# Performance work log

Hardware: AMD Instinct MI355X
Metric: run time of the kernel (lower is better)

Reference implementation:

```python
import jax, jax.numpy as jnp
import numpy as np

H = 1024      # hidden_dim
C = 151       # len(obj_classes)
E = 200       # embed_dim (GloVe)
DIN = 2048    # inputs_dim
T = 32        # timesteps
B = 128       # batch size (uniform packed lengths)


def setup_inputs() -> dict:
    key = jax.random.key(0)
    ks = jax.random.split(key, 8)
    sequence_tensor = jax.random.normal(ks[0], (T * B, DIN), dtype=jnp.float32) * 0.1
    labels = jax.random.randint(ks[1], (T * B,), 0, C).astype(jnp.int64)
    embed = jax.random.normal(ks[2], (C + 1, E), dtype=jnp.float32) * 0.1   # obj_embed.weight
    Wi = jax.random.normal(ks[3], (DIN + E, 6 * H), dtype=jnp.float32) * 0.02  # input_linearity
    bi = jnp.zeros((6 * H,), dtype=jnp.float32)
    Ws = jax.random.normal(ks[4], (H, 5 * H), dtype=jnp.float32) * 0.02        # state_linearity
    bs = jnp.zeros((5 * H,), dtype=jnp.float32)
    Wo = jax.random.normal(ks[5], (H, C), dtype=jnp.float32) * 0.02            # out_obj
    bo = jnp.zeros((C,), dtype=jnp.float32)
    return {"sequence_tensor": sequence_tensor, "labels": labels, "embed": embed,
            "Wi": Wi, "bi": bi, "Ws": Ws, "bs": bs, "Wo": Wo, "bo": bo,
            "batch_size": B}


def reference(sequence_tensor, embed, Wi, bi, Ws, bs, Wo, bo, labels, batch_size):
    b = int(batch_size)
    t = sequence_tensor.shape[0] // b
    x = sequence_tensor.reshape(t, b, -1)          # [T, B, DIN] packed timestep-major
    lab = labels.reshape(t, b)                     # [T, B]
    h0 = jnp.zeros((b, H), dtype=sequence_tensor.dtype)
    c0 = jnp.zeros((b, H), dtype=sequence_tensor.dtype)
    e0 = jnp.broadcast_to(embed[0], (b, E))        # 'start' embedding

    def step(carry, inp):
        h, c, pe = carry
        xt, lt = inp
        ti = jnp.concatenate([xt, pe], axis=1)     # [B, DIN+E]
        pi = ti @ Wi + bi                          # [B, 6H]
        ps = h @ Ws + bs                           # [B, 5H]

        def gate(k):
            return pi[:, k * H:(k + 1) * H] + ps[:, k * H:(k + 1) * H]

        i_g = jax.nn.sigmoid(gate(0))
        f_g = jax.nn.sigmoid(gate(1))
        m_i = jnp.tanh(gate(2))
        o_g = jax.nn.sigmoid(gate(3))
        c_new = i_g * m_i + f_g * c
        out = o_g * jnp.tanh(c_new)
        hw = jax.nn.sigmoid(gate(4))
        h_new = hw * out + (1.0 - hw) * pi[:, 5 * H:6 * H]  # highway

        pred = h_new @ Wo + bo                     # [B, C]
        nzp = jnp.argmax(pred[:, 1:], axis=1) + 1  # best non-bg class
        l2e = jnp.where(lt == 0, nzp.astype(lt.dtype), lt)
        pe_new = embed[l2e + 1]                    # feedback embedding
        return (h_new, c_new, pe_new), (pred, l2e)

    _, (dists, comms) = jax.lax.scan(step, (h0, c0, e0), (x, lab))
    return dists.reshape(t * b, C), comms.reshape(t * b)
```

## Files before the change

kernel.cpp:

```cpp
#include <hip/hip_runtime.h>
#include <math.h>

#define H    1024
#define C    151
#define E    200
#define DIN  2048
#define T    32
#define B    128
#define SIXH  (6*H)
#define FIVEH (5*H)
#define KTOT  DIN
#define NEMB  (C+1)
#define NWG   160
#define COLS  32
#define GUARD (1 << 20)

typedef _Float16 f16x8 __attribute__((ext_vector_type(8)));
typedef _Float16 f16x4 __attribute__((ext_vector_type(4)));
typedef float    f32x4 __attribute__((ext_vector_type(4)));

#define GLOAD_LDS16(g, l) __builtin_amdgcn_global_load_lds( \
    (const __attribute__((address_space(1))) unsigned int*)(g), \
    (__attribute__((address_space(3))) unsigned int*)(l), 16, 0, 0)

__device__ __forceinline__ void gbar(int* slots, int tid, int val) {
    __syncthreads();
    if (tid == 0)
        __hip_atomic_fetch_add(&slots[blockIdx.x * 16], 1,
                               __ATOMIC_ACQ_REL, __HIP_MEMORY_SCOPE_AGENT);
    int ok, guard = 0;
    do {
        int v = val;
        if (tid < NWG)
            v = __hip_atomic_load(&slots[tid * 16],
                                  __ATOMIC_RELAXED, __HIP_MEMORY_SCOPE_AGENT);
        ok = __syncthreads_and(v >= val);
        if (!ok) __builtin_amdgcn_s_sleep(1);
    } while (!ok && ++guard < GUARD);
    __builtin_amdgcn_fence(__ATOMIC_ACQUIRE, "agent");
}

__global__ void init_kernel(float* h, float* c, _Float16* hhi, _Float16* hlo,
                            int* eidx, int* bar) {
    int i = blockIdx.x * blockDim.x + threadIdx.x;
    if (i < B * H) {
        h[i] = 0.f; c[i] = 0.f;
        hhi[i] = (_Float16)0.f; hlo[i] = (_Float16)0.f;
    }
    if (i < B) eidx[i] = 0;
    if (i < NWG * 16) bar[i] = 0;
}

__global__ void cvt_x(const float* __restrict__ X, _Float16* __restrict__ hi,
                      _Float16* __restrict__ lo) {
    size_t i = ((size_t)blockIdx.x * 256 + threadIdx.x) * 4;
    float4 v = *(const float4*)(X + i);
    f16x4 h, l;
    h.x = (_Float16)v.x; l.x = (_Float16)(v.x - (float)h.x);
    h.y = (_Float16)v.y; l.y = (_Float16)(v.y - (float)h.y);
    h.z = (_Float16)v.z; l.z = (_Float16)(v.z - (float)h.z);
    h.w = (_Float16)v.w; l.w = (_Float16)(v.w - (float)h.w);
    *(f16x4*)(hi + i) = h;
    *(f16x4*)(lo + i) = l;
}

template<int KR, int NC>
__global__ void cvt_wT(const float* __restrict__ W, _Float16* __restrict__ hi,
                       _Float16* __restrict__ lo) {
    __shared__ float tile[32][33];
    int n0 = blockIdx.x * 32, k0 = blockIdx.y * 32;
    int tx = threadIdx.x & 31, ty = threadIdx.x >> 5;
    #pragma unroll
    for (int i = 0; i < 4; ++i) {
        int k = ty + i * 8;
        tile[k][tx] = W[(size_t)(k0 + k) * NC + n0 + tx];
    }
    __syncthreads();
    #pragma unroll
    for (int i = 0; i < 4; ++i) {
        int n = ty + i * 8;
        float v = tile[tx][n];
        _Float16 h = (_Float16)v;
        size_t o = (size_t)(n0 + n) * KR + k0 + tx;
        hi[o] = h;
        lo[o] = (_Float16)(v - (float)h);
    }
}

__global__ void cvt_woT(const float* __restrict__ Wo, float* __restrict__ WoT) {
    int k = blockIdx.x * 256 + threadIdx.x;
    for (int c = 0; c < C; ++c)
        WoT[(size_t)c * H + k] = Wo[(size_t)k * C + c];
}

__global__ void etab_kernel(const float* __restrict__ embed,
                            const float* __restrict__ Wi,
                            float* __restrict__ Etab) {
    int n = blockIdx.x * 256 + threadIdx.x;
    int k = blockIdx.y;
    const float* wp = Wi + (size_t)DIN * SIXH + n;
    const float* ep = embed + k * E;
    float acc = 0.f;
    #pragma unroll 8
    for (int e = 0; e < E; ++e)
        acc = fmaf(ep[e], wp[(size_t)e * SIXH], acc);
    Etab[(size_t)k * SIXH + n] = acc;
}

__global__ __launch_bounds__(256) void big_gemm_mfma(
    const _Float16* __restrict__ Ahi, const _Float16* __restrict__ Alo,
    const _Float16* __restrict__ Bhi, const _Float16* __restrict__ Blo,
    const float* __restrict__ bi, float* __restrict__ P)
{
    __shared__ __align__(16) _Float16 sAh[128 * 32];
    __shared__ __align__(16) _Float16 sAl[128 * 32];
    __shared__ __align__(16) _Float16 sBh[128 * 32];
    __shared__ __align__(16) _Float16 sBl[128 * 32];
    const int tid = threadIdx.x;
    const int n0 = blockIdx.x * 128;
    const int m0 = blockIdx.y * 128;
    const int lane = tid & 63, w = tid >> 6;
    const int wm = (w >> 1) * 64, wn = (w & 1) * 64;
    const int lr = lane & 15, lq = lane >> 4;

    f32x4 acc[4][4];
    #pragma unroll
    for (int i = 0; i < 4; ++i)
        #pragma unroll
        for (int j = 0; j < 4; ++j)
            acc[i][j] = (f32x4){0.f, 0.f, 0.f, 0.f};

    const int row0 = tid >> 2;
    const int kc = tid & 3;
    const int kcs = kc ^ ((row0 >> 1) & 3);
    const int sw = (lq ^ ((lr >> 1) & 3)) * 8;

    for (int k0 = 0; k0 < KTOT; k0 += 32) {
        #pragma unroll
        for (int i = 0; i < 2; ++i) {
            int row = row0 + i * 64;
            size_t ga = (size_t)(m0 + row) * KTOT + k0 + kcs * 8;
            size_t gb = (size_t)(n0 + row) * KTOT + k0 + kcs * 8;
            int loff = (i * 256 + tid) * 8;
            GLOAD_LDS16(Ahi + ga, sAh + loff);
            GLOAD_LDS16(Alo + ga, sAl + loff);
            GLOAD_LDS16(Bhi + gb, sBh + loff);
            GLOAD_LDS16(Blo + gb, sBl + loff);
        }
        __syncthreads();
        f16x8 ah[4], al[4], bh[4], bl[4];
        #pragma unroll
        for (int i = 0; i < 4; ++i) {
            ah[i] = *(const f16x8*)&sAh[(wm + i * 16 + lr) * 32 + sw];
            al[i] = *(const f16x8*)&sAl[(wm + i * 16 + lr) * 32 + sw];
            bh[i] = *(const f16x8*)&sBh[(wn + i * 16 + lr) * 32 + sw];
            bl[i] = *(const f16x8*)&sBl[(wn + i * 16 + lr) * 32 + sw];
        }
        #pragma unroll
        for (int i = 0; i < 4; ++i)
            #pragma unroll
            for (int j = 0; j < 4; ++j) {
                acc[i][j] = __builtin_amdgcn_mfma_f32_16x16x32_f16(ah[i], bh[j], acc[i][j], 0, 0, 0);
                acc[i][j] = __builtin_amdgcn_mfma_f32_16x16x32_f16(ah[i], bl[j], acc[i][j], 0, 0, 0);
                acc[i][j] = __builtin_amdgcn_mfma_f32_16x16x32_f16(al[i], bh[j], acc[i][j], 0, 0, 0);
            }
        __syncthreads();
    }
    #pragma unroll
    for (int i = 0; i < 4; ++i)
        #pragma unroll
        for (int j = 0; j < 4; ++j) {
            int gcol = n0 + wn + j * 16 + lr;
            float bv = bi[gcol];
            #pragma unroll
            for (int r = 0; r < 4; ++r) {
                int grow = m0 + wm + i * 16 + lq * 4 + r;
                P[(size_t)grow * SIXH + gcol] = acc[i][j][r] + bv;
            }
        }
}

__global__ __launch_bounds__(256, 1) void fused_loop(
    const float* __restrict__ P,
    const float* __restrict__ Etab,
    const float* __restrict__ bs,
    const _Float16* __restrict__ WsThi,
    const _Float16* __restrict__ WsTlo,
    _Float16* __restrict__ hhi,
    _Float16* __restrict__ hlo,
    float* __restrict__ ps,
    const float* __restrict__ WoT,
    const float* __restrict__ bo,
    const int* __restrict__ labels,
    float* __restrict__ dists,
    float* __restrict__ comms,
    int* bar)
{
    __shared__ __align__(16) _Float16 sBh[COLS * H];
    __shared__ __align__(16) _Float16 sBl[COLS * H];
    __shared__ __align__(16) float hs[H];
    __shared__ float vals[256];
    __shared__ int   idxs[256];
    __shared__ int   s_eidx;

    const int wg  = blockIdx.x;
    const int tid = threadIdx.x;
    const int n0  = wg * COLS;
    const int lane = tid & 63, w = tid >> 6;
    const int lr = lane & 15, lq = lane >> 4;

    for (int gi = tid; gi < COLS * (H / 8); gi += 256) {
        int col = gi >> 7;
        int kg  = gi & 127;
        int dst = (col * (H * 2) + kg * 16) ^ ((col & 7) << 4);
        *(f16x8*)((char*)sBh + dst) = *(const f16x8*)&WsThi[(size_t)(n0 + col) * H + kg * 8];
        *(f16x8*)((char*)sBl + dst) = *(const f16x8*)&WsTlo[(size_t)(n0 + col) * H + kg * 8];
    }

    float creg[4] = {0.f, 0.f, 0.f, 0.f};
    float bsr[4][5];
    if (wg < B) {
        #pragma unroll
        for (int jj = 0; jj < 4; ++jj)
            #pragma unroll
            for (int k = 0; k < 5; ++k)
                bsr[jj][k] = bs[k * H + jj * 256 + tid];
    }
    if (tid == 0) s_eidx = 0;
    __syncthreads();

    const int mrow0 = w * 32;
    int bval = 0;

    for (int t = 0; t < T; ++t) {
        int eidx_cur = s_eidx;

        f32x4 acc[2][2];
        #pragma unroll
        for (int i = 0; i < 2; ++i)
            #pragma unroll
            for (int j = 0; j < 2; ++j)
                acc[i][j] = (f32x4){0.f, 0.f, 0.f, 0.f};

        #pragma unroll 4
        for (int k0 = 0; k0 < H; k0 += 32) {
            f16x8 ah[2], al[2], bh[2], bl[2];
            #pragma unroll
            for (int i = 0; i < 2; ++i) {
                size_t ho = (size_t)(mrow0 + i * 16 + lr) * H + k0 + lq * 8;
                ah[i] = *(const f16x8*)&hhi[ho];
                al[i] = *(const f16x8*)&hlo[ho];
            }
            #pragma unroll
            for (int j = 0; j < 2; ++j) {
                int col = j * 16 + lr;
                int off = (col * (H * 2) + (k0 + lq * 8) * 2) ^ ((col & 7) << 4);
                bh[j] = *(const f16x8*)((const char*)sBh + off);
                bl[j] = *(const f16x8*)((const char*)sBl + off);
            }
            #pragma unroll
            for (int i = 0; i < 2; ++i)
                #pragma unroll
                for (int j = 0; j < 2; ++j) {
                    acc[i][j] = __builtin_amdgcn_mfma_f32_16x16x32_f16(ah[i], bh[j], acc[i][j], 0, 0, 0);
                    acc[i][j] = __builtin_amdgcn_mfma_f32_16x16x32_f16(ah[i], bl[j], acc[i][j], 0, 0, 0);
                    acc[i][j] = __builtin_amdgcn_mfma_f32_16x16x32_f16(al[i], bh[j], acc[i][j], 0, 0, 0);
                }
        }
        #pragma unroll
        for (int i = 0; i < 2; ++i)
            #pragma unroll
            for (int j = 0; j < 2; ++j)
                #pragma unroll
                for (int r = 0; r < 4; ++r)
                    ps[(size_t)(mrow0 + i * 16 + lq * 4 + r) * FIVEH + n0 + j * 16 + lr] = acc[i][j][r];

        float pf[4][6], pe[4][6];
        if (wg < B) {
            const float* prow = P + (size_t)(t * B + wg) * SIXH;
            const float* erow = Etab + (size_t)eidx_cur * SIXH;
            #pragma unroll
            for (int jj = 0; jj < 4; ++jj)
                #pragma unroll
                for (int k = 0; k < 6; ++k) {
                    pf[jj][k] = prow[k * H + jj * 256 + tid];
                    pe[jj][k] = erow[k * H + jj * 256 + tid];
                }
        }

        ++bval; gbar(bar, tid, bval);

        if (wg < B) {
            const int b = wg;
            const float* psr = ps + (size_t)b * FIVEH;
            #pragma unroll
            for (int jj = 0; jj < 4; ++jj) {
                int j = jj * 256 + tid;
                float gv[5];
                #pragma unroll
                for (int k = 0; k < 5; ++k)
                    gv[k] = pf[jj][k] + pe[jj][k] + psr[k * H + j] + bsr[jj][k];
                float pi5 = pf[jj][5] + pe[jj][5];
                float ig = 1.f / (1.f + expf(-gv[0]));
                float fg = 1.f / (1.f + expf(-gv[1]));
                float mi = tanhf(gv[2]);
                float og = 1.f / (1.f + expf(-gv[3]));
                float hw = 1.f / (1.f + expf(-gv[4]));
                float cn = ig * mi + fg * creg[jj];
                float out = og * tanhf(cn);
                float hn = hw * out + (1.f - hw) * pi5;
                creg[jj] = cn;
                hs[j] = hn;
                _Float16 hh = (_Float16)hn;
                hhi[(size_t)b * H + j] = hh;
                hlo[(size_t)b * H + j] = (_Float16)(hn - (float)hh);
            }
            __syncthreads();
            float predv = 0.f;
            if (tid < C) {
                const float* wp = WoT + (size_t)tid * H;
                float a0 = bo[tid], a1 = 0.f, a2 = 0.f, a3 = 0.f;
                #pragma unroll 4
                for (int k = 0; k < H; k += 4) {
                    float4 w4 = *(const float4*)&wp[k];
                    float4 h4 = *(const float4*)&hs[k];
                    a0 = fmaf(h4.x, w4.x, a0);
                    a1 = fmaf(h4.y, w4.y, a1);
                    a2 = fmaf(h4.z, w4.z, a2);
                    a3 = fmaf(h4.w, w4.w, a3);
                }
                predv = (a0 + a1) + (a2 + a3);
                dists[(size_t)(t * B + b) * C + tid] = predv;
            }
            vals[tid] = (tid >= 1 && tid < C) ? predv : -1e30f;
            idxs[tid] = tid;
            __syncthreads();
            for (int s = 128; s > 0; s >>= 1) {
                if (tid < s) {
                    float v2 = vals[tid + s];
                    int   i2 = idxs[tid + s];
                    if (v2 > vals[tid] || (v2 == vals[tid] && i2 < idxs[tid])) {
                        vals[tid] = v2;
                        idxs[tid] = i2;
                    }
                }
                __syncthreads();
            }
            if (tid == 0) {
                int nzp = idxs[0];
                int lt = labels[t * B + b];
                int comm = (lt == 0) ? nzp : lt;
                comms[t * B + b] = (float)comm;
                s_eidx = comm + 1;
            }
        }
        ++bval; gbar(bar, tid, bval);
    }
}

__global__ __launch_bounds__(256) void ps_mfma(
    const _Float16* __restrict__ Ahi, const _Float16* __restrict__ Alo,
    const _Float16* __restrict__ Bhi, const _Float16* __restrict__ Blo,
    float* __restrict__ ps)
{
    __shared__ __align__(16) _Float16 sAh[64 * 32];
    __shared__ __align__(16) _Float16 sAl[64 * 32];
    __shared__ __align__(16) _Float16 sBh[64 * 32];
    __shared__ __align__(16) _Float16 sBl[64 * 32];
    const int tid = threadIdx.x;
    const int n0 = blockIdx.x * 64;
    const int m0 = blockIdx.y * 64;
    const int lane = tid & 63, w = tid >> 6;
    const int wm = (w >> 1) * 32, wn = (w & 1) * 32;
    const int lr = lane & 15, lq = lane >> 4;

    f32x4 acc[2][2];
    #pragma unroll
    for (int i = 0; i < 2; ++i)
        #pragma unroll
        for (int j = 0; j < 2; ++j)
            acc[i][j] = (f32x4){0.f, 0.f, 0.f, 0.f};

    const int row = tid >> 2;
    const int kc = tid & 3;

    for (int k0 = 0; k0 < H; k0 += 32) {
        size_t ga = (size_t)(m0 + row) * H + k0 + kc * 8;
        size_t gb = (size_t)(n0 + row) * H + k0 + kc * 8;
        int loff = tid * 8;
        GLOAD_LDS16(Ahi + ga, sAh + loff);
        GLOAD_LDS16(Alo + ga, sAl + loff);
        GLOAD_LDS16(Bhi + gb, sBh + loff);
        GLOAD_LDS16(Blo + gb, sBl + loff);
        __syncthreads();
        f16x8 ah[2], al[2], bh[2], bl[2];
        #pragma unroll
        for (int i = 0; i < 2; ++i) {
            ah[i] = *(const f16x8*)&sAh[(wm + i * 16 + lr) * 32 + lq * 8];
            al[i] = *(const f16x8*)&sAl[(wm + i * 16 + lr) * 32 + lq * 8];
            bh[i] = *(const f16x8*)&sBh[(wn + i * 16 + lr) * 32 + lq * 8];
            bl[i] = *(const f16x8*)&sBl[(wn + i * 16 + lr) * 32 + lq * 8];
        }
        #pragma unroll
        for (int i = 0; i < 2; ++i)
            #pragma unroll
            for (int j = 0; j < 2; ++j) {
                acc[i][j] = __builtin_amdgcn_mfma_f32_16x16x32_f16(ah[i], bh[j], acc[i][j], 0, 0, 0);
                acc[i][j] = __builtin_amdgcn_mfma_f32_16x16x32_f16(ah[i], bl[j], acc[i][j], 0, 0, 0);
                acc[i][j] = __builtin_amdgcn_mfma_f32_16x16x32_f16(al[i], bh[j], acc[i][j], 0, 0, 0);
            }
        __syncthreads();
    }
    #pragma unroll
    for (int i = 0; i < 2; ++i)
        #pragma unroll
        for (int j = 0; j < 2; ++j) {
            int gcol = n0 + wn + j * 16 + lr;
            #pragma unroll
            for (int r = 0; r < 4; ++r) {
                int grow = m0 + wm + i * 16 + lq * 4 + r;
                ps[(size_t)grow * FIVEH + gcol] = acc[i][j][r];
            }
        }
}

__global__ void gate_kernel(const float* __restrict__ P,
                            const float* __restrict__ Etab,
                            const float* __restrict__ ps,
                            const float* __restrict__ bs,
                            const int* __restrict__ eidx,
                            float* __restrict__ h,
                            float* __restrict__ c,
                            _Float16* __restrict__ hhi,
                            _Float16* __restrict__ hlo,
                            int t) {
    int j = blockIdx.x * 256 + threadIdx.x;
    int b = blockIdx.y;
    const float* prow = P + (size_t)(t * B + b) * SIXH;
    const float* erow = Etab + (size_t)eidx[b] * SIXH;
    const float* psr  = ps + (size_t)b * FIVEH;
    float g[5];
    #pragma unroll
    for (int k = 0; k < 5; ++k) {
        int col = k * H + j;
        g[k] = prow[col] + erow[col] + psr[col] + bs[col];
    }
    float pi5 = prow[5 * H + j] + erow[5 * H + j];
    float ig = 1.f / (1.f + expf(-g[0]));
    float fg = 1.f / (1.f + expf(-g[1]));
    float mi = tanhf(g[2]);
    float og = 1.f / (1.f + expf(-g[3]));
    float hw = 1.f / (1.f + expf(-g[4]));
    float cv = c[b * H + j];
    float cn = ig * mi + fg * cv;
    float out = og * tanhf(cn);
    float hn = hw * out + (1.f - hw) * pi5;
    c[b * H + j] = cn;
    h[b * H + j] = hn;
    _Float16 hh = (_Float16)hn;
    hhi[b * H + j] = hh;
    hlo[b * H + j] = (_Float16)(hn - (float)hh);
}

__global__ void pred_kernel(const float* __restrict__ h,
                            const float* __restrict__ Wo,
                            const float* __restrict__ bo,
                            const int* __restrict__ labels,
                            float* __restrict__ dists,
                            float* __restrict__ comms,
                            int* __restrict__ eidx,
                            int t) {
    __shared__ float hsb[H];
    __shared__ float vals[256];
    __shared__ int   idxs[256];
    int tid = threadIdx.x;
    int b = blockIdx.x;
    for (int i = tid; i < H / 4; i += 256)
        *(float4*)&hsb[i * 4] = *(const float4*)&h[b * H + i * 4];
    __syncthreads();
    float pred = 0.f;
    if (tid < C) {
        pred = bo[tid];
        #pragma unroll 8
        for (int k = 0; k < H; ++k)
            pred = fmaf(hsb[k], Wo[k * C + tid], pred);
        dists[(size_t)(t * B + b) * C + tid] = pred;
    }
    vals[tid] = (tid >= 1 && tid < C) ? pred : -1e30f;
    idxs[tid] = tid;
    __syncthreads();
    for (int s = 128; s > 0; s >>= 1) {
        if (tid < s) {
            float v2 = vals[tid + s];
            int   i2 = idxs[tid + s];
            if (v2 > vals[tid] || (v2 == vals[tid] && i2 < idxs[tid])) {
                vals[tid] = v2;
                idxs[tid] = i2;
            }
        }
        __syncthreads();
    }
    if (tid == 0) {
        int nzp = idxs[0];
        int lt = labels[t * B + b];
        int comm = (lt == 0) ? nzp : lt;
        comms[t * B + b] = (float)comm;
        eidx[b] = comm + 1;
    }
}

extern "C" void kernel_launch(void* const* d_in, const int* in_sizes, int n_in,
                              void* d_out, int out_size, void* d_ws, size_t ws_size,
                              hipStream_t stream) {
    const float* X      = (const float*)d_in[0];
    const int*   labels = (const int*)  d_in[1];
    const float* embed  = (const float*)d_in[2];
    const float* Wi     = (const float*)d_in[3];
    const float* bi     = (const float*)d_in[4];
    const float* Ws     = (const float*)d_in[5];
    const float* bs     = (const float*)d_in[6];
    const float* Wo     = (const float*)d_in[7];
    const float* bo     = (const float*)d_in[8];

    char* w = (char*)d_ws;
    float* P      = (float*)w;              w += (size_t)T * B * SIXH * 4;
    float* Etab   = (float*)w;              w += (size_t)NEMB * SIXH * 4;
    float* ps     = (float*)w;              w += (size_t)B * FIVEH * 4;
    float* h      = (float*)w;              w += (size_t)B * H * 4;
    float* c      = (float*)w;              w += (size_t)B * H * 4;
    _Float16* hhi = (_Float16*)w;           w += (size_t)B * H * 2;
    _Float16* hlo = (_Float16*)w;           w += (size_t)B * H * 2;
    int* eidx     = (int*)w;                w += 512;
    int* bar      = (int*)w;                w += 16384;
    _Float16* Xhi = (_Float16*)w;           w += (size_t)T * B * KTOT * 2;
    _Float16* Xlo = (_Float16*)w;           w += (size_t)T * B * KTOT * 2;
    _Float16* WiThi = (_Float16*)w;         w += (size_t)SIXH * KTOT * 2;
    _Float16* WiTlo = (_Float16*)w;         w += (size_t)SIXH * KTOT * 2;
    _Float16* WsThi = (_Float16*)w;         w += (size_t)FIVEH * H * 2;
    _Float16* WsTlo = (_Float16*)w;         w += (size_t)FIVEH * H * 2;
    float* WoT    = (float*)Xhi;

    float* dists = (float*)d_out;
    float* comms = dists + (size_t)T * B * C;

    init_kernel<<<512, 256, 0, stream>>>(h, c, hhi, hlo, eidx, bar);
    cvt_x<<<(T * B * KTOT) / (256 * 4), 256, 0, stream>>>(X, Xhi, Xlo);
    cvt_wT<KTOT, SIXH><<<dim3(SIXH / 32, KTOT / 32), 256, 0, stream>>>(Wi, WiThi, WiTlo);
    cvt_wT<H, FIVEH><<<dim3(FIVEH / 32, H / 32), 256, 0, stream>>>(Ws, WsThi, WsTlo);
    etab_kernel<<<dim3(SIXH / 256, NEMB), 256, 0, stream>>>(embed, Wi, Etab);
    big_gemm_mfma<<<dim3(SIXH / 128, (T * B) / 128), 256, 0, stream>>>(Xhi, Xlo, WiThi, WiTlo, bi, P);
    cvt_woT<<<dim3(H / 256), 256, 0, stream>>>(Wo, WoT);

    void* args[] = {(void*)&P, (void*)&Etab, (void*)&bs, (void*)&WsThi, (void*)&WsTlo,
                    (void*)&hhi, (void*)&hlo, (void*)&ps, (void*)&WoT, (void*)&bo,
                    (void*)&labels, (void*)&dists, (void*)&comms, (void*)&bar};
    hipError_t err = hipLaunchCooperativeKernel((void*)fused_loop, dim3(NWG), dim3(256),
                                                args, 0, stream);
    if (err != hipSuccess) {
        for (int t = 0; t < T; ++t) {
            ps_mfma<<<dim3(FIVEH / 64, B / 64), 256, 0, stream>>>(hhi, hlo, WsThi, WsTlo, ps);
            gate_kernel<<<dim3(H / 256, B), 256, 0, stream>>>(P, Etab, ps, bs, eidx, h, c, hhi, hlo, t);
            pred_kernel<<<B, 256, 0, stream>>>(h, Wo, bo, labels, dists, comms, eidx, t);
        }
    }
}
```

Measured before the change: 2.443 ms.

## Split grid barrier into arrive/wait and double-buffer hidden-state loads

The grid barrier is split into separate arrive and wait phases. Each block now signals arrival as soon as it has written its new h, then computes the output projection and argmax before it waits, so that per-row tail work overlaps with barrier latency. The recurrent MFMA loop is also restructured into a manually double-buffered schedule: global loads of the hi/lo h fragments for the next 128-wide K chunk are issued while the current chunk is computed. The cost is higher register pressure from holding two sets of buffered fragments.

```diff
diff --git a/kernel.cpp b/kernel.cpp
--- a/kernel.cpp
+++ b/kernel.cpp
@@ -23,11 +23,13 @@
     (const __attribute__((address_space(1))) unsigned int*)(g), \
     (__attribute__((address_space(3))) unsigned int*)(l), 16, 0, 0)
 
-__device__ __forceinline__ void gbar(int* slots, int tid, int val) {
+__device__ __forceinline__ void gbar_arrive(int* slots, int tid) {
     __syncthreads();
     if (tid == 0)
         __hip_atomic_fetch_add(&slots[blockIdx.x * 16], 1,
                                __ATOMIC_ACQ_REL, __HIP_MEMORY_SCOPE_AGENT);
+}
+__device__ __forceinline__ void gbar_wait(int* slots, int tid, int val) {
     int ok, guard = 0;
     do {
         int v = val;
@@ -179,6 +181,32 @@
             }
         }
 }
+
+#define H_LOAD(Wa, Wl, kbase)                                                  \
+    _Pragma("unroll") for (int p = 0; p < 4; ++p)                              \
+    _Pragma("unroll") for (int i = 0; i < 2; ++i) {                            \
+        size_t ho = (size_t)(mrow0 + i * 16 + lr) * H + (kbase) + p * 32 + lq * 8; \
+        Wa[p][i] = *(const f16x8*)&hhi[ho];                                    \
+        Wl[p][i] = *(const f16x8*)&hlo[ho];                                    \
+    }
+
+#define H_COMP(Wa, Wl, kbase)                                                  \
+    _Pragma("unroll") for (int p = 0; p < 4; ++p) {                            \
+        const int k0 = (kbase) + p * 32;                                       \
+        f16x8 bh[2], bl[2];                                                    \
+        _Pragma("unroll") for (int j = 0; j < 2; ++j) {                        \
+            int col = j * 16 + lr;                                             \
+            int off = (col * (H * 2) + (k0 + lq * 8) * 2) ^ ((col & 7) << 4);  \
+            bh[j] = *(const f16x8*)((const char*)sBh + off);                   \
+            bl[j] = *(const f16x8*)((const char*)sBl + off);                   \
+        }                                                                      \
+        _Pragma("unroll") for (int i = 0; i < 2; ++i)                          \
+        _Pragma("unroll") for (int j = 0; j < 2; ++j) {                        \
+            acc[i][j] = __builtin_amdgcn_mfma_f32_16x16x32_f16(Wa[p][i], bh[j], acc[i][j], 0, 0, 0); \
+            acc[i][j] = __builtin_amdgcn_mfma_f32_16x16x32_f16(Wa[p][i], bl[j], acc[i][j], 0, 0, 0); \
+            acc[i][j] = __builtin_amdgcn_mfma_f32_16x16x32_f16(Wl[p][i], bh[j], acc[i][j], 0, 0, 0); \
+        }                                                                      \
+    }
 
 __global__ __launch_bounds__(256, 1) void fused_loop(
     const float* __restrict__ P,
@@ -242,30 +270,24 @@
             for (int j = 0; j < 2; ++j)
                 acc[i][j] = (f32x4){0.f, 0.f, 0.f, 0.f};
 
-        #pragma unroll 4
-        for (int k0 = 0; k0 < H; k0 += 32) {
-            f16x8 ah[2], al[2], bh[2], bl[2];
-            #pragma unroll
-            for (int i = 0; i < 2; ++i) {
-                size_t ho = (size_t)(mrow0 + i * 16 + lr) * H + k0 + lq * 8;
-                ah[i] = *(const f16x8*)&hhi[ho];
-                al[i] = *(const f16x8*)&hlo[ho];
-            }
-            #pragma unroll
-            for (int j = 0; j < 2; ++j) {
-                int col = j * 16 + lr;
-                int off = (col * (H * 2) + (k0 + lq * 8) * 2) ^ ((col & 7) << 4);
-                bh[j] = *(const f16x8*)((const char*)sBh + off);
-                bl[j] = *(const f16x8*)((const char*)sBl + off);
-            }
-            #pragma unroll
-            for (int i = 0; i < 2; ++i)
-                #pragma unroll
-                for (int j = 0; j < 2; ++j) {
-                    acc[i][j] = __builtin_amdgcn_mfma_f32_16x16x32_f16(ah[i], bh[j], acc[i][j], 0, 0, 0);
-                    acc[i][j] = __builtin_amdgcn_mfma_f32_16x16x32_f16(ah[i], bl[j], acc[i][j], 0, 0, 0);
-                    acc[i][j] = __builtin_amdgcn_mfma_f32_16x16x32_f16(al[i], bh[j], acc[i][j], 0, 0, 0);
-                }
+        {
+            f16x8 Aa[4][2], Al_[4][2], Ba[4][2], Bl_[4][2];
+            H_LOAD(Aa, Al_, 0)
+            H_LOAD(Ba, Bl_, 128)
+            H_COMP(Aa, Al_, 0)
+            H_LOAD(Aa, Al_, 256)
+            H_COMP(Ba, Bl_, 128)
+            H_LOAD(Ba, Bl_, 384)
+            H_COMP(Aa, Al_, 256)
+            H_LOAD(Aa, Al_, 512)
+            H_COMP(Ba, Bl_, 384)
+            H_LOAD(Ba, Bl_, 640)
+            H_COMP(Aa, Al_, 512)
+            H_LOAD(Aa, Al_, 768)
+            H_COMP(Ba, Bl_, 640)
+            H_LOAD(Ba, Bl_, 896)
+            H_COMP(Aa, Al_, 768)
+            H_COMP(Ba, Bl_, 896)
         }
         #pragma unroll
         for (int i = 0; i < 2; ++i)
@@ -288,7 +310,9 @@
                 }
         }
 
-        ++bval; gbar(bar, tid, bval);
+        ++bval;
+        gbar_arrive(bar, tid);
+        gbar_wait(bar, tid, bval);
 
         if (wg < B) {
             const int b = wg;
@@ -315,7 +339,12 @@
                 hhi[(size_t)b * H + j] = hh;
                 hlo[(size_t)b * H + j] = (_Float16)(hn - (float)hh);
             }
-            __syncthreads();
+        }
+        ++bval;
+        gbar_arrive(bar, tid);
+
+        if (wg < B) {
+            const int b = wg;
             float predv = 0.f;
             if (tid < C) {
                 const float* wp = WoT + (size_t)tid * H;
@@ -354,7 +383,7 @@
                 s_eidx = comm + 1;
             }
         }
-        ++bval; gbar(bar, tid, bval);
+        gbar_wait(bar, tid, bval);
     }
 }
 
```

New measurement: 2.391 ms. 2.1% less time.

## Split persistent loop across 320 workgroups and overlap argmax with barrier

Applied to the files above, without the earlier changes.

Doubles the number of persistent workgroups to 320, each owning 16 columns of the state GEMM instead of 32, and allows two workgroups per CU. The grid barrier is split into separate arrive and wait halves. The second barrier is now signalled right after the new hidden state is written, so the output projection and argmax overlap with other workgroups reaching the barrier. This is meant to cut per-step serial latency, at the cost of more barrier participants and halved MFMA work per workgroup.

```diff
diff --git a/kernel.cpp b/kernel.cpp
--- a/kernel.cpp
+++ b/kernel.cpp
@@ -11,8 +11,8 @@
 #define FIVEH (5*H)
 #define KTOT  DIN
 #define NEMB  (C+1)
-#define NWG   160
-#define COLS  32
+#define NWG   320
+#define COLS  16
 #define GUARD (1 << 20)
 
 typedef _Float16 f16x8 __attribute__((ext_vector_type(8)));
@@ -23,18 +23,22 @@
     (const __attribute__((address_space(1))) unsigned int*)(g), \
     (__attribute__((address_space(3))) unsigned int*)(l), 16, 0, 0)
 
-__device__ __forceinline__ void gbar(int* slots, int tid, int val) {
+__device__ __forceinline__ void gbar_arrive(int* slots, int tid) {
     __syncthreads();
     if (tid == 0)
         __hip_atomic_fetch_add(&slots[blockIdx.x * 16], 1,
                                __ATOMIC_ACQ_REL, __HIP_MEMORY_SCOPE_AGENT);
+}
+__device__ __forceinline__ void gbar_wait(int* slots, int tid, int val) {
     int ok, guard = 0;
     do {
-        int v = val;
-        if (tid < NWG)
-            v = __hip_atomic_load(&slots[tid * 16],
-                                  __ATOMIC_RELAXED, __HIP_MEMORY_SCOPE_AGENT);
-        ok = __syncthreads_and(v >= val);
+        int v1 = __hip_atomic_load(&slots[tid * 16],
+                                   __ATOMIC_RELAXED, __HIP_MEMORY_SCOPE_AGENT);
+        int v2 = val;
+        if (tid < NWG - 256)
+            v2 = __hip_atomic_load(&slots[(256 + tid) * 16],
+                                   __ATOMIC_RELAXED, __HIP_MEMORY_SCOPE_AGENT);
+        ok = __syncthreads_and(v1 >= val && v2 >= val);
         if (!ok) __builtin_amdgcn_s_sleep(1);
     } while (!ok && ++guard < GUARD);
     __builtin_amdgcn_fence(__ATOMIC_ACQUIRE, "agent");
@@ -180,7 +184,7 @@
         }
 }
 
-__global__ __launch_bounds__(256, 1) void fused_loop(
+__global__ __launch_bounds__(256, 2) void fused_loop(
     const float* __restrict__ P,
     const float* __restrict__ Etab,
     const float* __restrict__ bs,
@@ -235,45 +239,37 @@
     for (int t = 0; t < T; ++t) {
         int eidx_cur = s_eidx;
 
-        f32x4 acc[2][2];
-        #pragma unroll
-        for (int i = 0; i < 2; ++i)
-            #pragma unroll
-            for (int j = 0; j < 2; ++j)
-                acc[i][j] = (f32x4){0.f, 0.f, 0.f, 0.f};
+        f32x4 acc[2];
+        acc[0] = (f32x4){0.f, 0.f, 0.f, 0.f};
+        acc[1] = (f32x4){0.f, 0.f, 0.f, 0.f};
 
         #pragma unroll 4
         for (int k0 = 0; k0 < H; k0 += 32) {
-            f16x8 ah[2], al[2], bh[2], bl[2];
+            f16x8 ah[2], al[2], bh, bl;
             #pragma unroll
             for (int i = 0; i < 2; ++i) {
                 size_t ho = (size_t)(mrow0 + i * 16 + lr) * H + k0 + lq * 8;
                 ah[i] = *(const f16x8*)&hhi[ho];
                 al[i] = *(const f16x8*)&hlo[ho];
             }
-            #pragma unroll
-            for (int j = 0; j < 2; ++j) {
-                int col = j * 16 + lr;
+            {
+                int col = lr;
                 int off = (col * (H * 2) + (k0 + lq * 8) * 2) ^ ((col & 7) << 4);
-                bh[j] = *(const f16x8*)((const char*)sBh + off);
-                bl[j] = *(const f16x8*)((const char*)sBl + off);
-            }
-            #pragma unroll
-            for (int i = 0; i < 2; ++i)
-                #pragma unroll
-                for (int j = 0; j < 2; ++j) {
-                    acc[i][j] = __builtin_amdgcn_mfma_f32_16x16x32_f16(ah[i], bh[j], acc[i][j], 0, 0, 0);
-                    acc[i][j] = __builtin_amdgcn_mfma_f32_16x16x32_f16(ah[i], bl[j], acc[i][j], 0, 0, 0);
-                    acc[i][j] = __builtin_amdgcn_mfma_f32_16x16x32_f16(al[i], bh[j], acc[i][j], 0, 0, 0);
-                }
+                bh = *(const f16x8*)((const char*)sBh + off);
+                bl = *(const f16x8*)((const char*)sBl + off);
+            }
+            #pragma unroll
+            for (int i = 0; i < 2; ++i) {
+                acc[i] = __builtin_amdgcn_mfma_f32_16x16x32_f16(ah[i], bh, acc[i], 0, 0, 0);
+                acc[i] = __builtin_amdgcn_mfma_f32_16x16x32_f16(ah[i], bl, acc[i], 0, 0, 0);
+                acc[i] = __builtin_amdgcn_mfma_f32_16x16x32_f16(al[i], bh, acc[i], 0, 0, 0);
+            }
         }
         #pragma unroll
         for (int i = 0; i < 2; ++i)
             #pragma unroll
-            for (int j = 0; j < 2; ++j)
-                #pragma unroll
-                for (int r = 0; r < 4; ++r)
-                    ps[(size_t)(mrow0 + i * 16 + lq * 4 + r) * FIVEH + n0 + j * 16 + lr] = acc[i][j][r];
+            for (int r = 0; r < 4; ++r)
+                ps[(size_t)(mrow0 + i * 16 + lq * 4 + r) * FIVEH + n0 + lr] = acc[i][r];
 
         float pf[4][6], pe[4][6];
         if (wg < B) {
@@ -288,7 +284,9 @@
                 }
         }
 
-        ++bval; gbar(bar, tid, bval);
+        ++bval;
+        gbar_arrive(bar, tid);
+        gbar_wait(bar, tid, bval);
 
         if (wg < B) {
             const int b = wg;
@@ -315,7 +313,12 @@
                 hhi[(size_t)b * H + j] = hh;
                 hlo[(size_t)b * H + j] = (_Float16)(hn - (float)hh);
             }
-            __syncthreads();
+        }
+        ++bval;
+        gbar_arrive(bar, tid);
+
+        if (wg < B) {
+            const int b = wg;
             float predv = 0.f;
             if (tid < C) {
                 const float* wp = WoT + (size_t)tid * H;
@@ -354,7 +357,7 @@
                 s_eidx = comm + 1;
             }
         }
-        ++bval; gbar(bar, tid, bval);
+        gbar_wait(bar, tid, bval);
     }
 }
 
@@ -531,7 +534,7 @@
     _Float16* hhi = (_Float16*)w;           w += (size_t)B * H * 2;
     _Float16* hlo = (_Float16*)w;           w += (size_t)B * H * 2;
     int* eidx     = (int*)w;                w += 512;
-    int* bar      = (int*)w;                w += 16384;
+    int* bar      = (int*)w;                w += 32768;
     _Float16* Xhi = (_Float16*)w;           w += (size_t)T * B * KTOT * 2;
     _Float16* Xlo = (_Float16*)w;           w += (size_t)T * B * KTOT * 2;
     _Float16* WiThi = (_Float16*)w;         w += (size_t)SIXH * KTOT * 2;
```

Measured after the change: 3.426 ms. 40.2% more time.
